# Kernel optimization log

Measured on AMD Instinct MI355X. Metric: run time of the kernel, lower is better.

## Reference

```python
import jax, jax.numpy as jnp
import numpy as np

B, I, H = 16384, 1024, 1024

def setup_inputs() -> dict:
    key = jax.random.key(0)
    ks = jax.random.split(key, 14)
    s_in = 1.0 / np.sqrt(I)
    s_h = 1.0 / np.sqrt(H)
    return {
        "x": jax.random.normal(ks[0], (B, I), jnp.float32),
        "h_prev": jax.random.normal(ks[1], (B, H), jnp.float32),
        "Wiz_w": jax.random.normal(ks[2], (H, I), jnp.float32) * s_in,
        "Wiz_b": jax.random.normal(ks[3], (H,), jnp.float32) * s_in,
        "Wir_w": jax.random.normal(ks[4], (H, I), jnp.float32) * s_in,
        "Wir_b": jax.random.normal(ks[5], (H,), jnp.float32) * s_in,
        "Wih_w": jax.random.normal(ks[6], (H, I), jnp.float32) * s_in,
        "Wih_b": jax.random.normal(ks[7], (H,), jnp.float32) * s_in,
        "Whz_w": jax.random.normal(ks[8], (H, H), jnp.float32) * s_h,
        "Whz_b": jax.random.normal(ks[9], (H,), jnp.float32) * s_h,
        "Whr_w": jax.random.normal(ks[10], (H, H), jnp.float32) * s_h,
        "Whr_b": jax.random.normal(ks[11], (H,), jnp.float32) * s_h,
        "Whh_w": jax.random.normal(ks[12], (H, H), jnp.float32) * s_h,
        "Whh_b": jax.random.normal(ks[13], (H,), jnp.float32) * s_h,
    }

def _linear(x, w, b):
    # torch nn.Linear: x @ w.T + b
    return jnp.dot(x, w.T) + b

def reference(x, h_prev, Wiz_w, Wiz_b, Wir_w, Wir_b, Wih_w, Wih_b,
              Whz_w, Whz_b, Whr_w, Whr_b, Whh_w, Whh_b):
    z = jax.nn.sigmoid(_linear(x, Wiz_w, Wiz_b) + _linear(h_prev, Whz_w, Whz_b))
    r = jax.nn.sigmoid(_linear(x, Wir_w, Wir_b) + _linear(h_prev, Whr_w, Whr_b))
    g = jnp.tanh(_linear(x, Wih_w, Wih_b) + r * _linear(h_prev, Whh_w, Whh_b))
    h_new = (1.0 - z) * g + z * h_prev
    return h_new
```

## Files before the change

### kernel.cpp

```cpp
#include <hip/hip_runtime.h>
#include <hip/hip_bf16.h>
#include <stdint.h>


#define BM 128
#define BN 128
#define BK 64
#define THREADS 512

typedef __bf16 bf16_t;
typedef __bf16 bf16x8 __attribute__((ext_vector_type(8)));
typedef float f32x4 __attribute__((ext_vector_type(4)));

#define XOFF 0
#define HOFF 16777216
#define WOFF 33554432
#define WSZ  1048576
#define TOTAL_ELEMS 39845888

__device__ __forceinline__ void gload16(const void* g, void* l) {
  __builtin_amdgcn_global_load_lds(
      (const __attribute__((address_space(1))) void*)g,
      (__attribute__((address_space(3))) void*)l, 16, 0, 0);
}

__device__ __forceinline__ float fast_sigmoid(float v) {
  return 1.0f / (1.0f + __expf(-v));
}
__device__ __forceinline__ float fast_tanh(float v) {
  float e = __expf(-2.0f * fabsf(v));
  float t = (1.0f - e) / (1.0f + e);
  return v < 0.0f ? -t : t;
}

__global__ __launch_bounds__(256) void convert_bf16(
    const float* __restrict__ x, const float* __restrict__ h,
    const float* __restrict__ wiz, const float* __restrict__ wir,
    const float* __restrict__ wih, const float* __restrict__ whz,
    const float* __restrict__ whr, const float* __restrict__ whh,
    bf16_t* __restrict__ ws)
{
  const long total8 = TOTAL_ELEMS / 8;
  long i = (long)blockIdx.x * blockDim.x + threadIdx.x;
  const long stride = (long)gridDim.x * blockDim.x;
  for (; i < total8; i += stride) {
    long e = i * 8;
    const float* src;
    if (e < HOFF) src = x + e;
    else if (e < WOFF) src = h + (e - HOFF);
    else {
      long r = e - WOFF;
      int wi = (int)(r >> 20);
      long off = r & (WSZ - 1);
      const float* wp = (wi == 0) ? wiz : (wi == 1) ? wir : (wi == 2) ? wih
                       : (wi == 3) ? whz : (wi == 4) ? whr : whh;
      src = wp + off;
    }
    float4 v0 = *(const float4*)src;
    float4 v1 = *(const float4*)(src + 4);
    bf16x8 o;
    o[0] = (__bf16)v0.x; o[1] = (__bf16)v0.y; o[2] = (__bf16)v0.z; o[3] = (__bf16)v0.w;
    o[4] = (__bf16)v1.x; o[5] = (__bf16)v1.y; o[6] = (__bf16)v1.z; o[7] = (__bf16)v1.w;
    *(bf16x8*)(ws + e) = o;
  }
}

__global__ __launch_bounds__(THREADS, 2) void gru_gemm(
    const bf16_t* __restrict__ ws,
    const float* __restrict__ h_prev,
    const float* __restrict__ biz, const float* __restrict__ bir,
    const float* __restrict__ bih, const float* __restrict__ bhz,
    const float* __restrict__ bhr, const float* __restrict__ bhh,
    float* __restrict__ out)
{
  extern __shared__ char smem[];
  const int tid = threadIdx.x;
  const int lane = tid & 63;
  const int wv = tid >> 6;
  const int wr = wv >> 2;
  const int wc = wv & 3;
  const int l15 = lane & 15, l4 = lane >> 4;

  const int id = blockIdx.x;
  const int swz = (id & 7) * 128 + (id >> 3);
  const int m0 = (swz & 127) * BM;
  const int n0 = (swz >> 7) * BN;

  const bf16_t* xbf  = ws + XOFF;
  const bf16_t* hbf  = ws + HOFF;
  const bf16_t* wizp = ws + WOFF + 0 * WSZ;
  const bf16_t* wirp = ws + WOFF + 1 * WSZ;
  const bf16_t* wihp = ws + WOFF + 2 * WSZ;
  const bf16_t* whzp = ws + WOFF + 3 * WSZ;
  const bf16_t* whrp = ws + WOFF + 4 * WSZ;
  const bf16_t* whhp = ws + WOFF + 5 * WSZ;

  const int rrow = tid >> 3;
  const int ksrc_e = (((tid & 7) ^ (rrow & 7)) << 3);
  const size_t aoff0 = (size_t)(m0 + rrow) * 1024 + ksrc_e;
  const size_t woff0 = (size_t)(n0 + rrow) * 1024 + ksrc_e;
  const int wlds = wv * 1024;

  int aoffs[4][2], woffs[2][2];
  #pragma unroll
  for (int mi = 0; mi < 4; ++mi) {
    int row = wr * 64 + mi * 16 + l15;
    int sw = (row & 7) << 4;
    #pragma unroll
    for (int ks = 0; ks < 2; ++ks) {
      int kb = ks * 64 + l4 * 16;
      aoffs[mi][ks] = row * 128 + (kb ^ sw);
    }
  }
  #pragma unroll
  for (int ni = 0; ni < 2; ++ni) {
    int row = wc * 32 + ni * 16 + l15;
    int sw = (row & 7) << 4;
    #pragma unroll
    for (int ks = 0; ks < 2; ++ks) {
      int kb = ks * 64 + l4 * 16;
      woffs[ni][ks] = row * 128 + (kb ^ sw);
    }
  }

  f32x4 accZ[4][2], accR[4][2], accGX[4][2], accGH[4][2];
  const f32x4 zero = {0.f, 0.f, 0.f, 0.f};
  #pragma unroll
  for (int mi = 0; mi < 4; ++mi)
    #pragma unroll
    for (int ni = 0; ni < 2; ++ni) {
      accZ[mi][ni] = zero; accR[mi][ni] = zero;
      accGX[mi][ni] = zero; accGH[mi][ni] = zero;
    }

  auto stage = [&](int bufp, int t) {
    const int kk = (t * BK) & 1023;
    const bool xh = (t < 16);
    const bf16_t* As = xh ? xbf : hbf;
    const bf16_t* W0 = xh ? wizp : whzp;
    const bf16_t* W1 = xh ? wirp : whrp;
    const bf16_t* W2 = xh ? wihp : whhp;
    char* base = smem + bufp * 65536;
    gload16(As + aoff0 + kk,         base + 0     + wlds);
    gload16(As + aoff0 + kk + 65536, base + 8192  + wlds);
    gload16(W0 + woff0 + kk,         base + 16384 + wlds);
    gload16(W0 + woff0 + kk + 65536, base + 24576 + wlds);
    gload16(W1 + woff0 + kk,         base + 32768 + wlds);
    gload16(W1 + woff0 + kk + 65536, base + 40960 + wlds);
    gload16(W2 + woff0 + kk,         base + 49152 + wlds);
    gload16(W2 + woff0 + kk + 65536, base + 57344 + wlds);
  };

  auto compute = [&](int bufp, f32x4 (&accG)[4][2]) {
    const char* lb = smem + bufp * 65536;
    #pragma unroll
    for (int ks = 0; ks < 2; ++ks) {
      bf16x8 a[4], b0[2], b1[2], b2[2];
      #pragma unroll
      for (int mi = 0; mi < 4; ++mi)
        a[mi] = *(const bf16x8*)(lb + aoffs[mi][ks]);
      #pragma unroll
      for (int ni = 0; ni < 2; ++ni) {
        b0[ni] = *(const bf16x8*)(lb + 16384 + woffs[ni][ks]);
        b1[ni] = *(const bf16x8*)(lb + 32768 + woffs[ni][ks]);
        b2[ni] = *(const bf16x8*)(lb + 49152 + woffs[ni][ks]);
      }
      #pragma unroll
      for (int mi = 0; mi < 4; ++mi)
        #pragma unroll
        for (int ni = 0; ni < 2; ++ni) {
          accZ[mi][ni] = __builtin_amdgcn_mfma_f32_16x16x32_bf16(a[mi], b0[ni], accZ[mi][ni], 0, 0, 0);
          accR[mi][ni] = __builtin_amdgcn_mfma_f32_16x16x32_bf16(a[mi], b1[ni], accR[mi][ni], 0, 0, 0);
          accG[mi][ni] = __builtin_amdgcn_mfma_f32_16x16x32_bf16(a[mi], b2[ni], accG[mi][ni], 0, 0, 0);
        }
    }
  };

  int buf = 0;
  stage(0, 0);
  __syncthreads();
  #pragma unroll 1
  for (int t = 0; t < 16; ++t) {
    stage(buf ^ 1, t + 1);
    compute(buf, accGX);
    __syncthreads();
    buf ^= 1;
  }
  #pragma unroll 1
  for (int t = 16; t < 32; ++t) {
    if (t + 1 < 32) stage(buf ^ 1, t + 1);
    compute(buf, accGH);
    __syncthreads();
    buf ^= 1;
  }

  #pragma unroll
  for (int ni = 0; ni < 2; ++ni) {
    const int n_g = n0 + wc * 32 + ni * 16 + l15;
    const float bz  = biz[n_g] + bhz[n_g];
    const float br  = bir[n_g] + bhr[n_g];
    const float bgx = bih[n_g];
    const float bgh = bhh[n_g];
    #pragma unroll
    for (int mi = 0; mi < 4; ++mi) {
      const int mrow = m0 + wr * 64 + mi * 16 + l4 * 4;
      #pragma unroll
      for (int j = 0; j < 4; ++j) {
        const size_t idx = (size_t)(mrow + j) * 1024 + n_g;
        const float z = fast_sigmoid(accZ[mi][ni][j] + bz);
        const float r = fast_sigmoid(accR[mi][ni][j] + br);
        const float g = fast_tanh(accGX[mi][ni][j] + bgx + r * (accGH[mi][ni][j] + bgh));
        out[idx] = (1.0f - z) * g + z * h_prev[idx];
      }
    }
  }
}

extern "C" void kernel_launch(void* const* d_in, const int* in_sizes, int n_in,
                              void* d_out, int out_size, void* d_ws, size_t ws_size,
                              hipStream_t stream) {
  (void)in_sizes; (void)n_in; (void)out_size; (void)ws_size;
  const float* x     = (const float*)d_in[0];
  const float* hprev = (const float*)d_in[1];
  const float* Wiz_w = (const float*)d_in[2];
  const float* Wiz_b = (const float*)d_in[3];
  const float* Wir_w = (const float*)d_in[4];
  const float* Wir_b = (const float*)d_in[5];
  const float* Wih_w = (const float*)d_in[6];
  const float* Wih_b = (const float*)d_in[7];
  const float* Whz_w = (const float*)d_in[8];
  const float* Whz_b = (const float*)d_in[9];
  const float* Whr_w = (const float*)d_in[10];
  const float* Whr_b = (const float*)d_in[11];
  const float* Whh_w = (const float*)d_in[12];
  const float* Whh_b = (const float*)d_in[13];
  float* out = (float*)d_out;
  bf16_t* ws = (bf16_t*)d_ws;

  hipFuncSetAttribute(reinterpret_cast<const void*>(gru_gemm),
                      hipFuncAttributeMaxDynamicSharedMemorySize, 131072);

  convert_bf16<<<2048, 256, 0, stream>>>(x, hprev, Wiz_w, Wir_w, Wih_w,
                                         Whz_w, Whr_w, Whh_w, ws);
  gru_gemm<<<1024, THREADS, 131072, stream>>>(ws, hprev, Wiz_b, Wir_b, Wih_b,
                                              Whz_b, Whr_b, Whh_b, out);
}
```

Before: 409.7 us.

## Interleave split async LDS prefetch with per-gate MFMA groups using explicit waitcnt

Splits each stage's global-to-LDS loads into three parts, one per weight gate, and issues them between the gate-wise MFMA groups rather than all at once before the compute. It replaces __syncthreads with an explicit vmcnt wait plus raw barriers and sched_barrier fences, and raises wave priority around the MFMA bursts. The aim is to overlap memory traffic with matrix math and avoid draining the whole load queue each step. The risk is in the hand-written vmcnt counts and barrier placement, and in the higher register pressure from holding all A fragments across both k-substeps.

```diff
diff --git a/kernel.cpp b/kernel.cpp
--- a/kernel.cpp
+++ b/kernel.cpp
@@ -107,20 +107,16 @@
     int row = wr * 64 + mi * 16 + l15;
     int sw = (row & 7) << 4;
     #pragma unroll
-    for (int ks = 0; ks < 2; ++ks) {
-      int kb = ks * 64 + l4 * 16;
-      aoffs[mi][ks] = row * 128 + (kb ^ sw);
-    }
+    for (int ks = 0; ks < 2; ++ks)
+      aoffs[mi][ks] = row * 128 + ((ks * 64 + l4 * 16) ^ sw);
   }
   #pragma unroll
   for (int ni = 0; ni < 2; ++ni) {
     int row = wc * 32 + ni * 16 + l15;
     int sw = (row & 7) << 4;
     #pragma unroll
-    for (int ks = 0; ks < 2; ++ks) {
-      int kb = ks * 64 + l4 * 16;
-      woffs[ni][ks] = row * 128 + (kb ^ sw);
-    }
+    for (int ks = 0; ks < 2; ++ks)
+      woffs[ni][ks] = row * 128 + ((ks * 64 + l4 * 16) ^ sw);
   }
 
   f32x4 accZ[4][2], accR[4][2], accGX[4][2], accGH[4][2];
@@ -133,66 +129,117 @@
       accGX[mi][ni] = zero; accGH[mi][ni] = zero;
     }
 
-  auto stage = [&](int bufp, int t) {
+  auto srcs = [&](int t, const bf16_t*& As, const bf16_t*& W0,
+                  const bf16_t*& W1, const bf16_t*& W2) {
+    const bool xh = (t < 16);
+    As = xh ? xbf : hbf;
+    W0 = xh ? wizp : whzp;
+    W1 = xh ? wirp : whrp;
+    W2 = xh ? wihp : whhp;
+  };
+  auto part0 = [&](int bufp, int t) {
     const int kk = (t * BK) & 1023;
-    const bool xh = (t < 16);
-    const bf16_t* As = xh ? xbf : hbf;
-    const bf16_t* W0 = xh ? wizp : whzp;
-    const bf16_t* W1 = xh ? wirp : whrp;
-    const bf16_t* W2 = xh ? wihp : whhp;
+    const bf16_t *As, *W0, *W1, *W2; srcs(t, As, W0, W1, W2);
     char* base = smem + bufp * 65536;
     gload16(As + aoff0 + kk,         base + 0     + wlds);
     gload16(As + aoff0 + kk + 65536, base + 8192  + wlds);
     gload16(W0 + woff0 + kk,         base + 16384 + wlds);
+  };
+  auto part1 = [&](int bufp, int t) {
+    const int kk = (t * BK) & 1023;
+    const bf16_t *As, *W0, *W1, *W2; srcs(t, As, W0, W1, W2);
+    char* base = smem + bufp * 65536;
     gload16(W0 + woff0 + kk + 65536, base + 24576 + wlds);
     gload16(W1 + woff0 + kk,         base + 32768 + wlds);
     gload16(W1 + woff0 + kk + 65536, base + 40960 + wlds);
+  };
+  auto part2 = [&](int bufp, int t) {
+    const int kk = (t * BK) & 1023;
+    const bf16_t *As, *W0, *W1, *W2; srcs(t, As, W0, W1, W2);
+    char* base = smem + bufp * 65536;
     gload16(W2 + woff0 + kk,         base + 49152 + wlds);
     gload16(W2 + woff0 + kk + 65536, base + 57344 + wlds);
   };
 
-  auto compute = [&](int bufp, f32x4 (&accG)[4][2]) {
-    const char* lb = smem + bufp * 65536;
-    #pragma unroll
-    for (int ks = 0; ks < 2; ++ks) {
-      bf16x8 a[4], b0[2], b1[2], b2[2];
+  auto kstep = [&](int t, f32x4 (&accG)[4][2], bool last) {
+    const int c = t & 1;
+    const char* lb = smem + c * 65536;
+    if (!last) {
+      part0(c ^ 1, t + 1);
+      asm volatile("s_waitcnt vmcnt(3)" ::: "memory");
+    } else {
+      asm volatile("s_waitcnt vmcnt(0)" ::: "memory");
+    }
+    __builtin_amdgcn_s_barrier();
+    __builtin_amdgcn_sched_barrier(0);
+    bf16x8 a[4][2];
+    #pragma unroll
+    for (int mi = 0; mi < 4; ++mi)
+      #pragma unroll
+      for (int ks = 0; ks < 2; ++ks)
+        a[mi][ks] = *(const bf16x8*)(lb + aoffs[mi][ks]);
+    {
+      bf16x8 b[2][2];
+      #pragma unroll
+      for (int ni = 0; ni < 2; ++ni)
+        #pragma unroll
+        for (int ks = 0; ks < 2; ++ks)
+          b[ni][ks] = *(const bf16x8*)(lb + 16384 + woffs[ni][ks]);
+      __builtin_amdgcn_s_setprio(1);
       #pragma unroll
       for (int mi = 0; mi < 4; ++mi)
-        a[mi] = *(const bf16x8*)(lb + aoffs[mi][ks]);
-      #pragma unroll
-      for (int ni = 0; ni < 2; ++ni) {
-        b0[ni] = *(const bf16x8*)(lb + 16384 + woffs[ni][ks]);
-        b1[ni] = *(const bf16x8*)(lb + 32768 + woffs[ni][ks]);
-        b2[ni] = *(const bf16x8*)(lb + 49152 + woffs[ni][ks]);
-      }
+        #pragma unroll
+        for (int ni = 0; ni < 2; ++ni)
+          #pragma unroll
+          for (int ks = 0; ks < 2; ++ks)
+            accZ[mi][ni] = __builtin_amdgcn_mfma_f32_16x16x32_bf16(a[mi][ks], b[ni][ks], accZ[mi][ni], 0, 0, 0);
+      __builtin_amdgcn_s_setprio(0);
+    }
+    if (!last) part1(c ^ 1, t + 1);
+    {
+      bf16x8 b[2][2];
+      #pragma unroll
+      for (int ni = 0; ni < 2; ++ni)
+        #pragma unroll
+        for (int ks = 0; ks < 2; ++ks)
+          b[ni][ks] = *(const bf16x8*)(lb + 32768 + woffs[ni][ks]);
+      __builtin_amdgcn_s_setprio(1);
       #pragma unroll
       for (int mi = 0; mi < 4; ++mi)
         #pragma unroll
-        for (int ni = 0; ni < 2; ++ni) {
-          accZ[mi][ni] = __builtin_amdgcn_mfma_f32_16x16x32_bf16(a[mi], b0[ni], accZ[mi][ni], 0, 0, 0);
-          accR[mi][ni] = __builtin_amdgcn_mfma_f32_16x16x32_bf16(a[mi], b1[ni], accR[mi][ni], 0, 0, 0);
-          accG[mi][ni] = __builtin_amdgcn_mfma_f32_16x16x32_bf16(a[mi], b2[ni], accG[mi][ni], 0, 0, 0);
-        }
-    }
-  };
-
-  int buf = 0;
-  stage(0, 0);
-  __syncthreads();
+        for (int ni = 0; ni < 2; ++ni)
+          #pragma unroll
+          for (int ks = 0; ks < 2; ++ks)
+            accR[mi][ni] = __builtin_amdgcn_mfma_f32_16x16x32_bf16(a[mi][ks], b[ni][ks], accR[mi][ni], 0, 0, 0);
+      __builtin_amdgcn_s_setprio(0);
+    }
+    if (!last) part2(c ^ 1, t + 1);
+    {
+      bf16x8 b[2][2];
+      #pragma unroll
+      for (int ni = 0; ni < 2; ++ni)
+        #pragma unroll
+        for (int ks = 0; ks < 2; ++ks)
+          b[ni][ks] = *(const bf16x8*)(lb + 49152 + woffs[ni][ks]);
+      __builtin_amdgcn_s_setprio(1);
+      #pragma unroll
+      for (int mi = 0; mi < 4; ++mi)
+        #pragma unroll
+        for (int ni = 0; ni < 2; ++ni)
+          #pragma unroll
+          for (int ks = 0; ks < 2; ++ks)
+            accG[mi][ni] = __builtin_amdgcn_mfma_f32_16x16x32_bf16(a[mi][ks], b[ni][ks], accG[mi][ni], 0, 0, 0);
+      __builtin_amdgcn_s_setprio(0);
+    }
+    __builtin_amdgcn_s_barrier();
+    __builtin_amdgcn_sched_barrier(0);
+  };
+
+  part0(0, 0); part1(0, 0); part2(0, 0);
   #pragma unroll 1
-  for (int t = 0; t < 16; ++t) {
-    stage(buf ^ 1, t + 1);
-    compute(buf, accGX);
-    __syncthreads();
-    buf ^= 1;
-  }
+  for (int t = 0; t < 16; ++t) kstep(t, accGX, false);
   #pragma unroll 1
-  for (int t = 16; t < 32; ++t) {
-    if (t + 1 < 32) stage(buf ^ 1, t + 1);
-    compute(buf, accGH);
-    __syncthreads();
-    buf ^= 1;
-  }
+  for (int t = 16; t < 32; ++t) kstep(t, accGH, t == 31);
 
   #pragma unroll
   for (int ni = 0; ni < 2; ++ni) {
```

After: 407.2 us. About the same (-0.6%).

## Switch GRU GEMM to 32x32x16 MFMA with explicit waitcnt pipelining

Applied to the files above, without the earlier changes.

The GEMM moves from 16x16x32 to 32x32x16 bf16 MFMA tiles, giving each wave 2x1 32x32 tiles with fewer LDS fragment loads per MFMA. The main loop is restructured to issue the next stage's global loads first, then wait with an explicit vmcnt count, use raw s_barrier, raise wave priority during the MFMA block and add a sched_barrier. The conversion kernel is also remapped to a fixed block-per-chunk layout without the grid-stride loop and branchy source selection. The hand-placed waitcnt and barrier choices depend on the compiler honouring the sched_barrier fencing, so getting them wrong could cause stalls or hazards.

```diff
diff --git a/kernel.cpp b/kernel.cpp
--- a/kernel.cpp
+++ b/kernel.cpp
@@ -10,13 +10,12 @@
 
 typedef __bf16 bf16_t;
 typedef __bf16 bf16x8 __attribute__((ext_vector_type(8)));
-typedef float f32x4 __attribute__((ext_vector_type(4)));
+typedef float f32x16 __attribute__((ext_vector_type(16)));
 
 #define XOFF 0
 #define HOFF 16777216
 #define WOFF 33554432
 #define WSZ  1048576
-#define TOTAL_ELEMS 39845888
 
 __device__ __forceinline__ void gload16(const void* g, void* l) {
   __builtin_amdgcn_global_load_lds(
@@ -31,6 +30,16 @@
   float e = __expf(-2.0f * fabsf(v));
   float t = (1.0f - e) / (1.0f + e);
   return v < 0.0f ? -t : t;
+}
+
+__device__ __forceinline__ void cvt8(const float* __restrict__ src,
+                                     bf16_t* __restrict__ dst) {
+  float4 v0 = *(const float4*)src;
+  float4 v1 = *(const float4*)(src + 4);
+  bf16x8 o;
+  o[0] = (__bf16)v0.x; o[1] = (__bf16)v0.y; o[2] = (__bf16)v0.z; o[3] = (__bf16)v0.w;
+  o[4] = (__bf16)v1.x; o[5] = (__bf16)v1.y; o[6] = (__bf16)v1.z; o[7] = (__bf16)v1.w;
+  *(bf16x8*)dst = o;
 }
 
 __global__ __launch_bounds__(256) void convert_bf16(
@@ -40,28 +49,28 @@
     const float* __restrict__ whr, const float* __restrict__ whh,
     bf16_t* __restrict__ ws)
 {
-  const long total8 = TOTAL_ELEMS / 8;
-  long i = (long)blockIdx.x * blockDim.x + threadIdx.x;
-  const long stride = (long)gridDim.x * blockDim.x;
-  for (; i < total8; i += stride) {
-    long e = i * 8;
-    const float* src;
-    if (e < HOFF) src = x + e;
-    else if (e < WOFF) src = h + (e - HOFF);
-    else {
-      long r = e - WOFF;
-      int wi = (int)(r >> 20);
-      long off = r & (WSZ - 1);
+  const int b = blockIdx.x, tid = threadIdx.x;
+  if (b < 2048) {
+    const float* src = (b < 1024) ? x : h;
+    bf16_t* dst = ws + ((b < 1024) ? XOFF : HOFF);
+    const long u0 = (long)(b & 1023) * 2048;
+    #pragma unroll
+    for (int j = 0; j < 8; ++j) {
+      long e = (u0 + (long)j * 256 + tid) * 8;
+      cvt8(src + e, dst + e);
+    }
+  } else {
+    const int wb = b - 2048;
+    const long u0 = (long)wb * 1536;
+    #pragma unroll
+    for (int j = 0; j < 6; ++j) {
+      long u = u0 + (long)j * 256 + tid;
+      int wi = (int)(u >> 17);
+      long off = (u & 131071) * 8;
       const float* wp = (wi == 0) ? wiz : (wi == 1) ? wir : (wi == 2) ? wih
                        : (wi == 3) ? whz : (wi == 4) ? whr : whh;
-      src = wp + off;
-    }
-    float4 v0 = *(const float4*)src;
-    float4 v1 = *(const float4*)(src + 4);
-    bf16x8 o;
-    o[0] = (__bf16)v0.x; o[1] = (__bf16)v0.y; o[2] = (__bf16)v0.z; o[3] = (__bf16)v0.w;
-    o[4] = (__bf16)v1.x; o[5] = (__bf16)v1.y; o[6] = (__bf16)v1.z; o[7] = (__bf16)v1.w;
-    *(bf16x8*)(ws + e) = o;
+      cvt8(wp + off, ws + WOFF + (long)wi * WSZ + off);
+    }
   }
 }
 
@@ -79,7 +88,7 @@
   const int wv = tid >> 6;
   const int wr = wv >> 2;
   const int wc = wv & 3;
-  const int l15 = lane & 15, l4 = lane >> 4;
+  const int l31 = lane & 31, lhi = lane >> 5;
 
   const int id = blockIdx.x;
   const int swz = (id & 7) * 128 + (id >> 3);
@@ -101,37 +110,29 @@
   const size_t woff0 = (size_t)(n0 + rrow) * 1024 + ksrc_e;
   const int wlds = wv * 1024;
 
-  int aoffs[4][2], woffs[2][2];
+  int aoffs[2][4], woffs[4];
   #pragma unroll
-  for (int mi = 0; mi < 4; ++mi) {
-    int row = wr * 64 + mi * 16 + l15;
+  for (int mi = 0; mi < 2; ++mi) {
+    int row = wr * 64 + mi * 32 + l31;
     int sw = (row & 7) << 4;
     #pragma unroll
-    for (int ks = 0; ks < 2; ++ks) {
-      int kb = ks * 64 + l4 * 16;
-      aoffs[mi][ks] = row * 128 + (kb ^ sw);
-    }
-  }
+    for (int ks = 0; ks < 4; ++ks)
+      aoffs[mi][ks] = row * 128 + ((ks * 32 + lhi * 16) ^ sw);
+  }
+  {
+    int row = wc * 32 + l31;
+    int sw = (row & 7) << 4;
+    #pragma unroll
+    for (int ks = 0; ks < 4; ++ks)
+      woffs[ks] = row * 128 + ((ks * 32 + lhi * 16) ^ sw);
+  }
+
+  f32x16 accZ[2], accR[2], accGX[2], accGH[2];
   #pragma unroll
-  for (int ni = 0; ni < 2; ++ni) {
-    int row = wc * 32 + ni * 16 + l15;
-    int sw = (row & 7) << 4;
-    #pragma unroll
-    for (int ks = 0; ks < 2; ++ks) {
-      int kb = ks * 64 + l4 * 16;
-      woffs[ni][ks] = row * 128 + (kb ^ sw);
-    }
-  }
-
-  f32x4 accZ[4][2], accR[4][2], accGX[4][2], accGH[4][2];
-  const f32x4 zero = {0.f, 0.f, 0.f, 0.f};
-  #pragma unroll
-  for (int mi = 0; mi < 4; ++mi)
-    #pragma unroll
-    for (int ni = 0; ni < 2; ++ni) {
-      accZ[mi][ni] = zero; accR[mi][ni] = zero;
-      accGX[mi][ni] = zero; accGH[mi][ni] = zero;
-    }
+  for (int mi = 0; mi < 2; ++mi) {
+    accZ[mi] = (f32x16)(0.f); accR[mi] = (f32x16)(0.f);
+    accGX[mi] = (f32x16)(0.f); accGH[mi] = (f32x16)(0.f);
+  }
 
   auto stage = [&](int bufp, int t) {
     const int kk = (t * BK) & 1023;
@@ -151,67 +152,61 @@
     gload16(W2 + woff0 + kk + 65536, base + 57344 + wlds);
   };
 
-  auto compute = [&](int bufp, f32x4 (&accG)[4][2]) {
-    const char* lb = smem + bufp * 65536;
-    #pragma unroll
-    for (int ks = 0; ks < 2; ++ks) {
-      bf16x8 a[4], b0[2], b1[2], b2[2];
-      #pragma unroll
-      for (int mi = 0; mi < 4; ++mi)
-        a[mi] = *(const bf16x8*)(lb + aoffs[mi][ks]);
-      #pragma unroll
-      for (int ni = 0; ni < 2; ++ni) {
-        b0[ni] = *(const bf16x8*)(lb + 16384 + woffs[ni][ks]);
-        b1[ni] = *(const bf16x8*)(lb + 32768 + woffs[ni][ks]);
-        b2[ni] = *(const bf16x8*)(lb + 49152 + woffs[ni][ks]);
-      }
-      #pragma unroll
-      for (int mi = 0; mi < 4; ++mi)
-        #pragma unroll
-        for (int ni = 0; ni < 2; ++ni) {
-          accZ[mi][ni] = __builtin_amdgcn_mfma_f32_16x16x32_bf16(a[mi], b0[ni], accZ[mi][ni], 0, 0, 0);
-          accR[mi][ni] = __builtin_amdgcn_mfma_f32_16x16x32_bf16(a[mi], b1[ni], accR[mi][ni], 0, 0, 0);
-          accG[mi][ni] = __builtin_amdgcn_mfma_f32_16x16x32_bf16(a[mi], b2[ni], accG[mi][ni], 0, 0, 0);
-        }
-    }
+  auto kstep = [&](int t, f32x16 (&accG)[2], bool last) {
+    const int c = t & 1;
+    const char* lb = smem + c * 65536;
+    if (!last) {
+      stage(c ^ 1, t + 1);
+      asm volatile("s_waitcnt vmcnt(8)" ::: "memory");
+    } else {
+      asm volatile("s_waitcnt vmcnt(0)" ::: "memory");
+    }
+    __builtin_amdgcn_s_barrier();
+    __builtin_amdgcn_sched_barrier(0);
+    bf16x8 a[2][4], bz[4], br[4], bg[4];
+    #pragma unroll
+    for (int ks = 0; ks < 4; ++ks) {
+      a[0][ks] = *(const bf16x8*)(lb + aoffs[0][ks]);
+      a[1][ks] = *(const bf16x8*)(lb + aoffs[1][ks]);
+      bz[ks]   = *(const bf16x8*)(lb + 16384 + woffs[ks]);
+      br[ks]   = *(const bf16x8*)(lb + 32768 + woffs[ks]);
+      bg[ks]   = *(const bf16x8*)(lb + 49152 + woffs[ks]);
+    }
+    __builtin_amdgcn_s_setprio(1);
+    #pragma unroll
+    for (int ks = 0; ks < 4; ++ks) {
+      accZ[0] = __builtin_amdgcn_mfma_f32_32x32x16_bf16(a[0][ks], bz[ks], accZ[0], 0, 0, 0);
+      accZ[1] = __builtin_amdgcn_mfma_f32_32x32x16_bf16(a[1][ks], bz[ks], accZ[1], 0, 0, 0);
+      accR[0] = __builtin_amdgcn_mfma_f32_32x32x16_bf16(a[0][ks], br[ks], accR[0], 0, 0, 0);
+      accR[1] = __builtin_amdgcn_mfma_f32_32x32x16_bf16(a[1][ks], br[ks], accR[1], 0, 0, 0);
+      accG[0] = __builtin_amdgcn_mfma_f32_32x32x16_bf16(a[0][ks], bg[ks], accG[0], 0, 0, 0);
+      accG[1] = __builtin_amdgcn_mfma_f32_32x32x16_bf16(a[1][ks], bg[ks], accG[1], 0, 0, 0);
+    }
+    __builtin_amdgcn_s_setprio(0);
+    __builtin_amdgcn_s_barrier();
   };
 
-  int buf = 0;
   stage(0, 0);
-  __syncthreads();
   #pragma unroll 1
-  for (int t = 0; t < 16; ++t) {
-    stage(buf ^ 1, t + 1);
-    compute(buf, accGX);
-    __syncthreads();
-    buf ^= 1;
-  }
+  for (int t = 0; t < 16; ++t) kstep(t, accGX, false);
   #pragma unroll 1
-  for (int t = 16; t < 32; ++t) {
-    if (t + 1 < 32) stage(buf ^ 1, t + 1);
-    compute(buf, accGH);
-    __syncthreads();
-    buf ^= 1;
-  }
-
+  for (int t = 16; t < 32; ++t) kstep(t, accGH, t == 31);
+
+  const int n_g = n0 + wc * 32 + l31;
+  const float bz  = biz[n_g] + bhz[n_g];
+  const float br  = bir[n_g] + bhr[n_g];
+  const float bgx = bih[n_g];
+  const float bgh = bhh[n_g];
   #pragma unroll
-  for (int ni = 0; ni < 2; ++ni) {
-    const int n_g = n0 + wc * 32 + ni * 16 + l15;
-    const float bz  = biz[n_g] + bhz[n_g];
-    const float br  = bir[n_g] + bhr[n_g];
-    const float bgx = bih[n_g];
-    const float bgh = bhh[n_g];
-    #pragma unroll
-    for (int mi = 0; mi < 4; ++mi) {
-      const int mrow = m0 + wr * 64 + mi * 16 + l4 * 4;
-      #pragma unroll
-      for (int j = 0; j < 4; ++j) {
-        const size_t idx = (size_t)(mrow + j) * 1024 + n_g;
-        const float z = fast_sigmoid(accZ[mi][ni][j] + bz);
-        const float r = fast_sigmoid(accR[mi][ni][j] + br);
-        const float g = fast_tanh(accGX[mi][ni][j] + bgx + r * (accGH[mi][ni][j] + bgh));
-        out[idx] = (1.0f - z) * g + z * h_prev[idx];
-      }
+  for (int mi = 0; mi < 2; ++mi) {
+    #pragma unroll
+    for (int reg = 0; reg < 16; ++reg) {
+      const int row_in = (reg & 3) + 8 * (reg >> 2) + 4 * lhi;
+      const size_t idx = (size_t)(m0 + wr * 64 + mi * 32 + row_in) * 1024 + n_g;
+      const float z = fast_sigmoid(accZ[mi][reg] + bz);
+      const float r = fast_sigmoid(accR[mi][reg] + br);
+      const float g = fast_tanh(accGX[mi][reg] + bgx + r * (accGH[mi][reg] + bgh));
+      out[idx] = (1.0f - z) * g + z * h_prev[idx];
     }
   }
 }
@@ -240,7 +235,7 @@
   hipFuncSetAttribute(reinterpret_cast<const void*>(gru_gemm),
                       hipFuncAttributeMaxDynamicSharedMemorySize, 131072);
 
-  convert_bf16<<<2048, 256, 0, stream>>>(x, hprev, Wiz_w, Wir_w, Wih_w,
+  convert_bf16<<<2560, 256, 0, stream>>>(x, hprev, Wiz_w, Wir_w, Wih_w,
                                          Whz_w, Whr_w, Whh_w, ws);
   gru_gemm<<<1024, THREADS, 131072, stream>>>(ws, hprev, Wiz_b, Wir_b, Wih_b,
                                               Whz_b, Whr_b, Whh_b, out);
```

After: 443.0 us. 8.1% more time.
